# Kernel optimization log

Hardware: AMD Instinct MI355X
Metric: run time of the kernel (lower is better)

## Reference

```python
import jax, jax.numpy as jnp
import numpy as np

B, S, H, NH = 2, 2048, 2048, 16
HD = H // NH  # 128
ROPE_BASE = 10000.0


def rotate_half(x):
    x1, x2 = x[..., : x.shape[-1] // 2], x[..., x.shape[-1] // 2 :]
    return jnp.concatenate((-x2, x1), axis=-1)


def rope_cos_sin(seq_len, dim, dtype):
    inv_freq = 1.0 / (ROPE_BASE ** (jnp.arange(0, dim, 2, dtype=jnp.float32) / dim))
    t = jnp.arange(seq_len, dtype=jnp.float32)
    freqs = jnp.einsum('i,j->ij', t, inv_freq)          # [S, dim/2]
    emb = jnp.concatenate((freqs, freqs), axis=-1)       # [S, dim]
    return jnp.cos(emb).astype(dtype), jnp.sin(emb).astype(dtype)


def setup_inputs() -> dict:
    key = jax.random.key(0)
    ks = jax.random.split(key, 5)
    std = 1.0 / np.sqrt(H)
    return {
        'hidden_states': jax.random.normal(ks[0], (B, S, H), dtype=jnp.float32),
        'Wq': jax.random.normal(ks[1], (H, H), dtype=jnp.float32) * std,
        'Wk': jax.random.normal(ks[2], (H, H), dtype=jnp.float32) * std,
        'Wv': jax.random.normal(ks[3], (H, H), dtype=jnp.float32) * std,
        'Wo': jax.random.normal(ks[4], (H, H), dtype=jnp.float32) * std,
    }


def reference(hidden_states, Wq, Wk, Wv, Wo):
    bsz, q_len, _ = hidden_states.shape
    scale = 1.0 / np.sqrt(HD)
    # QKV projections (nn.Linear: x @ W.T)
    q = (hidden_states @ Wq.T).reshape(bsz, q_len, NH, HD).transpose(0, 2, 1, 3)
    k = (hidden_states @ Wk.T).reshape(bsz, q_len, NH, HD).transpose(0, 2, 1, 3)
    v = (hidden_states @ Wv.T).reshape(bsz, q_len, NH, HD).transpose(0, 2, 1, 3)
    # RoPE
    cos, sin = rope_cos_sin(q_len, HD, hidden_states.dtype)  # [S, HD]
    cos = cos[None, None]
    sin = sin[None, None]
    q = q * cos + rotate_half(q) * sin
    k = k * cos + rotate_half(k) * sin
    # attention (no mask, eval dropout = identity)
    attn = jnp.einsum('bhqd,bhkd->bhqk', q, k) * scale
    attn = jax.nn.softmax(attn.astype(jnp.float32), axis=-1).astype(q.dtype)
    out = jnp.einsum('bhqk,bhkd->bhqd', attn, v)
    out = out.transpose(0, 2, 1, 3).reshape(bsz, q_len, H)
    return out @ Wo.T
```

## Files before the change

kernel.cpp:

```cpp
#include <hip/hip_runtime.h>
#include <hip/hip_bf16.h>
#include <math.h>

#define Bb 2
#define Ss 2048
#define Hh 2048
#define NHh 16
#define HDd 128
#define Mm (Bb*Ss)

typedef __bf16 bf16;
typedef __bf16 bf16x8 __attribute__((ext_vector_type(8)));
typedef __bf16 bf16x4 __attribute__((ext_vector_type(4)));
typedef float  f32x4  __attribute__((ext_vector_type(4)));

#define MFMA16(a,b,c) __builtin_amdgcn_mfma_f32_16x16x32_bf16((a),(b),(c),0,0,0)

__device__ __forceinline__ void gll16(const void* g, void* l) {
  __builtin_amdgcn_global_load_lds((__attribute__((address_space(1))) void*)g,
                                   (__attribute__((address_space(3))) void*)l, 16, 0, 0);
}

__global__ __launch_bounds__(256) void k_tables(float* __restrict__ cosT, float* __restrict__ sinT) {
  int id = blockIdx.x * 256 + threadIdx.x;
  int s = id >> 6, j = id & 63;
  float inv = 1.0f / powf(10000.0f, (float)j * (1.0f/64.0f));
  float a = (float)s * inv;
  cosT[id] = cosf(a);
  sinT[id] = sinf(a);
}

__global__ __launch_bounds__(256) void k_cvt(const float* __restrict__ in, bf16* __restrict__ out) {
  size_t i = ((size_t)blockIdx.x * 256 + threadIdx.x) * 4;
  float4 v = *(const float4*)(in + i);
  bf16x4 r = { (bf16)v.x, (bf16)v.y, (bf16)v.z, (bf16)v.w };
  *(bf16x4*)(out + i) = r;
}

template<int EPI>
__global__ __launch_bounds__(256) void k_gemm(
    const bf16* __restrict__ A, const bf16* __restrict__ Bw,
    float* __restrict__ C, bf16* __restrict__ QKb, bf16* __restrict__ Vt,
    int M, int N, int K)
{
  __shared__ bf16 As[128*64];
  __shared__ bf16 Bs[128*64];
  const int tid = threadIdx.x;
  const int lane = tid & 63;
  const int w = tid >> 6, wm = w & 1, wn = w >> 1;
  const int cpx = gridDim.x >> 3;
  const int bid = (blockIdx.x & 7) * cpx + (blockIdx.x >> 3);
  const int mt = M >> 7;
  const int bm = bid % mt, bn = bid / mt;
  const int r8 = tid >> 3, c8 = tid & 7;
  const bf16* Ag = A  + (size_t)(bm*128 + r8) * K + c8*8;
  const bf16* Bg = Bw + (size_t)(bn*128 + r8) * K + c8*8;
  bf16* Asw = &As[r8*64 + c8*8];
  bf16* Bsw = &Bs[r8*64 + c8*8];

  f32x4 acc[4][4] = {};
  for (int k0 = 0; k0 < K; k0 += 64) {
#pragma unroll
    for (int i = 0; i < 4; ++i) {
      gll16(Ag + (size_t)i*32*K + k0, Asw + i*32*64);
      gll16(Bg + (size_t)i*32*K + k0, Bsw + i*32*64);
    }
    __syncthreads();
#pragma unroll
    for (int kc = 0; kc < 2; ++kc) {
      bf16x8 af[4], bfv[4];
#pragma unroll
      for (int mi = 0; mi < 4; ++mi)
        af[mi] = *(const bf16x8*)&As[(wm*64 + mi*16 + (lane & 15))*64 + kc*32 + (lane>>4)*8];
#pragma unroll
      for (int ni = 0; ni < 4; ++ni)
        bfv[ni] = *(const bf16x8*)&Bs[(wn*64 + ni*16 + (lane & 15))*64 + kc*32 + (lane>>4)*8];
#pragma unroll
      for (int mi = 0; mi < 4; ++mi)
#pragma unroll
        for (int ni = 0; ni < 4; ++ni)
          acc[mi][ni] = MFMA16(af[mi], bfv[ni], acc[mi][ni]);
    }
    __syncthreads();
  }
  const int colB = bn*128 + wn*64;
  if (EPI == 0) {
#pragma unroll
    for (int mi = 0; mi < 4; ++mi)
#pragma unroll
      for (int ni = 0; ni < 4; ++ni) {
        int row0 = bm*128 + wm*64 + mi*16 + (lane>>4)*4;
        int col  = colB + ni*16 + (lane & 15);
#pragma unroll
        for (int r = 0; r < 4; ++r)
          C[(size_t)(row0 + r) * N + col] = acc[mi][ni][r];
      }
  } else if (colB < 4096) {
#pragma unroll
    for (int mi = 0; mi < 4; ++mi)
#pragma unroll
      for (int ni = 0; ni < 4; ++ni) {
        int row0 = bm*128 + wm*64 + mi*16 + (lane>>4)*4;
        int col  = colB + ni*16 + (lane & 15);
#pragma unroll
        for (int r = 0; r < 4; ++r)
          QKb[(size_t)(row0 + r) * 4096 + col] = (bf16)acc[mi][ni][r];
      }
  } else {
#pragma unroll
    for (int mi = 0; mi < 4; ++mi)
#pragma unroll
      for (int ni = 0; ni < 4; ++ni) {
        int row0 = bm*128 + wm*64 + mi*16 + (lane>>4)*4;
        int n2   = colB + ni*16 + (lane & 15) - 4096;
        int b = row0 >> 11, s0 = row0 & (Ss-1);
        bf16x4 pk = { (bf16)acc[mi][ni][0], (bf16)acc[mi][ni][1],
                      (bf16)acc[mi][ni][2], (bf16)acc[mi][ni][3] };
        *(bf16x4*)&Vt[((size_t)(b*NHh + (n2>>7))*HDd + (n2&127))*Ss + s0] = pk;
      }
  }
}

__global__ __launch_bounds__(256) void k_rope(
    const bf16* __restrict__ QKb,
    const float* __restrict__ cosT, const float* __restrict__ sinT,
    bf16* __restrict__ Qb, bf16* __restrict__ Kb)
{
  const size_t id = (size_t)blockIdx.x * 256 + threadIdx.x;
  const int j = (int)(id & 63);
  const size_t row = id >> 6;
  const size_t tok = row >> 4;
  const int h = (int)(row & 15);
  const int s = (int)(tok & (Ss - 1));
  const float c = cosT[s*64 + j], sn = sinT[s*64 + j];
  const size_t qbase = tok * 4096 + h * 128;
  const float scale = 0.08838834764831845f;
  float q1 = (float)QKb[qbase + j],        q2 = (float)QKb[qbase + 64 + j];
  float k1 = (float)QKb[qbase + 2048 + j], k2 = (float)QKb[qbase + 2048 + 64 + j];
  const size_t obase = row * HDd;
  Qb[obase + j]      = (bf16)((q1*c - q2*sn) * scale);
  Qb[obase + 64 + j] = (bf16)((q2*c + q1*sn) * scale);
  Kb[obase + j]      = (bf16)(k1*c - k2*sn);
  Kb[obase + 64 + j] = (bf16)(k2*c + k1*sn);
}

__global__ __launch_bounds__(256) void k_attn(
    const bf16* __restrict__ Qb, const bf16* __restrict__ Kb,
    const bf16* __restrict__ Vt, bf16* __restrict__ Ob)
{
  __shared__ bf16 Ks[2][64*128];
  __shared__ bf16 Vs[2][128*64];
  __shared__ bf16 Ps[64*72];
  const int cpx = gridDim.x >> 3;
  const int blk = (blockIdx.x & 7) * cpx + (blockIdx.x >> 3);
  const int bh = blk >> 5;
  const int q0 = (blk & 31) * 64;
  const int b = bh >> 4, h = bh & 15;
  const int tid = threadIdx.x, lane = tid & 63, w = tid >> 6;

  const int rK = tid >> 4, cK = tid & 15;
  const int rV = tid >> 3, cV = tid & 7;
  const bf16* Kg0 = Kb + ((size_t)b*Ss*NHh + h) * HDd;
  const bf16* Vg0 = Vt + (size_t)bh * HDd * Ss;

  auto stage = [&](int bufi, int kv0) {
#pragma unroll
    for (int i = 0; i < 4; ++i) {
      const int rowK = i*16 + rK; const int sck = cK ^ (rowK & 7);
      gll16(Kg0 + (size_t)(kv0 + rowK)*(NHh*HDd) + sck*8, &Ks[bufi][rowK*128 + cK*8]);
      const int rowV = i*32 + rV; const int scv = cV ^ (rowV & 7);
      gll16(Vg0 + (size_t)rowV*Ss + kv0 + scv*8, &Vs[bufi][rowV*64 + cV*8]);
    }
  };

  bf16x8 aq[4];
  {
    const int qr = q0 + w*16 + (lane & 15);
    const bf16* qp = Qb + ((size_t)(b*Ss + qr) * NHh + h) * HDd + (lane>>4)*8;
#pragma unroll
    for (int kc = 0; kc < 4; ++kc) aq[kc] = *(const bf16x8*)(qp + kc*32);
  }
  float m_i[4], l_i[4];
  f32x4 o[8] = {};
#pragma unroll
  for (int i = 0; i < 4; ++i) { m_i[i] = -1e30f; l_i[i] = 0.f; }

  stage(0, 0);
  asm volatile("s_waitcnt vmcnt(0)" ::: "memory");
  __builtin_amdgcn_s_barrier();
  asm volatile("" ::: "memory");

  const int NT = Ss / 64;
  for (int t = 0; t < NT; ++t) {
    const int cur = t & 1;
    if (t + 1 < NT) stage(cur ^ 1, (t + 1) * 64);

    f32x4 sf[4];
    __builtin_amdgcn_s_setprio(1);
#pragma unroll
    for (int nf = 0; nf < 4; ++nf) {
      f32x4 a = {0.f,0.f,0.f,0.f};
#pragma unroll
      for (int kc = 0; kc < 4; ++kc) {
        const int row = nf*16 + (lane & 15);
        const int ch  = kc*4 + (lane>>4);
        bf16x8 bk = *(const bf16x8*)&Ks[cur][row*128 + (ch ^ (row & 7))*8];
        a = MFMA16(aq[kc], bk, a);
      }
      sf[nf] = a;
    }
    __builtin_amdgcn_s_setprio(0);

    float x4[4];
#pragma unroll
    for (int i = 0; i < 4; ++i) {
      float x = fmaxf(fmaxf(sf[0][i], sf[1][i]), fmaxf(sf[2][i], sf[3][i]));
      x = fmaxf(x, __shfl_xor(x, 1));
      x = fmaxf(x, __shfl_xor(x, 2));
      x = fmaxf(x, __shfl_xor(x, 4));
      x = fmaxf(x, __shfl_xor(x, 8));
      x4[i] = x;
    }
    bool grow = (x4[0] > m_i[0] + 8.f) || (x4[1] > m_i[1] + 8.f) ||
                (x4[2] > m_i[2] + 8.f) || (x4[3] > m_i[3] + 8.f);
    if (__any(grow)) {
#pragma unroll
      for (int i = 0; i < 4; ++i) {
        float mnew = fmaxf(m_i[i], x4[i]);
        float c = __expf(m_i[i] - mnew);
        m_i[i] = mnew; l_i[i] *= c;
#pragma unroll
        for (int nfo = 0; nfo < 8; ++nfo) o[nfo][i] *= c;
      }
    }
    float ps[4] = {0.f,0.f,0.f,0.f};
#pragma unroll
    for (int nf = 0; nf < 4; ++nf)
#pragma unroll
      for (int i = 0; i < 4; ++i) {
        float pv = __expf(sf[nf][i] - m_i[i]);
        sf[nf][i] = pv;
        ps[i] += pv;
      }
#pragma unroll
    for (int i = 0; i < 4; ++i) {
      float s = ps[i];
      s += __shfl_xor(s, 1); s += __shfl_xor(s, 2);
      s += __shfl_xor(s, 4); s += __shfl_xor(s, 8);
      l_i[i] += s;
    }
#pragma unroll
    for (int nf = 0; nf < 4; ++nf)
#pragma unroll
      for (int i = 0; i < 4; ++i)
        Ps[(w*16 + (lane>>4)*4 + i)*72 + nf*16 + (lane & 15)] = (bf16)sf[nf][i];

    __builtin_amdgcn_s_setprio(1);
#pragma unroll
    for (int kc = 0; kc < 2; ++kc) {
      bf16x8 pa = *(const bf16x8*)&Ps[(w*16 + (lane & 15))*72 + kc*32 + (lane>>4)*8];
#pragma unroll
      for (int nfo = 0; nfo < 8; ++nfo) {
        const int row = nfo*16 + (lane & 15);
        const int ch  = kc*4 + (lane>>4);
        bf16x8 bv = *(const bf16x8*)&Vs[cur][row*64 + (ch ^ (row & 7))*8];
        o[nfo] = MFMA16(pa, bv, o[nfo]);
      }
    }
    __builtin_amdgcn_s_setprio(0);

    asm volatile("s_waitcnt vmcnt(0)" ::: "memory");
    __builtin_amdgcn_s_barrier();
    asm volatile("" ::: "memory");
  }

#pragma unroll
  for (int nfo = 0; nfo < 8; ++nfo)
#pragma unroll
    for (int i = 0; i < 4; ++i) {
      const int qr = q0 + w*16 + (lane>>4)*4 + i;
      const int d  = nfo*16 + (lane & 15);
      Ob[((size_t)(b*Ss + qr) * NHh + h) * HDd + d] = (bf16)(o[nfo][i] / l_i[i]);
    }
}

extern "C" void kernel_launch(void* const* d_in, const int* in_sizes, int n_in,
                              void* d_out, int out_size, void* d_ws, size_t ws_size,
                              hipStream_t stream) {
  (void)in_sizes; (void)n_in; (void)out_size; (void)ws_size;
  const float* X  = (const float*)d_in[0];
  const float* Wq = (const float*)d_in[1];
  const float* Wk = (const float*)d_in[2];
  const float* Wv = (const float*)d_in[3];
  const float* Wo = (const float*)d_in[4];
  float* out = (float*)d_out;

  char* p = (char*)d_ws;
  size_t off = 0;
  auto take = [&](size_t bytes) { char* r = p + off; off += (bytes + 255) & ~(size_t)255; return r; };

  float* cosT = (float*)take((size_t)Ss*64*4);
  float* sinT = (float*)take((size_t)Ss*64*4);
  bf16*  Xb   = (bf16*) take((size_t)Mm*Hh*2);
  bf16*  Wqkv = (bf16*) take((size_t)3*Hh*Hh*2);
  bf16*  Wob  = (bf16*) take((size_t)Hh*Hh*2);
  bf16*  QKb  = (bf16*) take((size_t)Mm*4096*2);
  bf16*  Vt   = (bf16*) take((size_t)Mm*Hh*2);
  bf16*  Qb   = (bf16*) take((size_t)Mm*Hh*2);
  bf16*  Kb2  = (bf16*) take((size_t)Mm*Hh*2);
  bf16*  Ob   = (bf16*) take((size_t)Mm*Hh*2);

  k_tables<<<(Ss*64)/256, 256, 0, stream>>>(cosT, sinT);
  k_cvt<<<(Mm*Hh)/4/256, 256, 0, stream>>>(X,  Xb);
  k_cvt<<<(Hh*Hh)/4/256, 256, 0, stream>>>(Wq, Wqkv);
  k_cvt<<<(Hh*Hh)/4/256, 256, 0, stream>>>(Wk, Wqkv + (size_t)Hh*Hh);
  k_cvt<<<(Hh*Hh)/4/256, 256, 0, stream>>>(Wv, Wqkv + (size_t)2*Hh*Hh);
  k_cvt<<<(Hh*Hh)/4/256, 256, 0, stream>>>(Wo, Wob);

  k_gemm<1><<<(Mm/128) * (3*Hh/128), 256, 0, stream>>>(Xb, Wqkv, nullptr, QKb, Vt, Mm, 3*Hh, Hh);
  k_rope<<<((size_t)Mm*NHh*64)/256, 256, 0, stream>>>(QKb, cosT, sinT, Qb, Kb2);
  k_attn<<<Bb*NHh*(Ss/64), 256, 0, stream>>>(Qb, Kb2, Vt, Ob);
  k_gemm<0><<<(Mm/128) * (Hh/128), 256, 0, stream>>>(Ob, Wob, out, nullptr, nullptr, Mm, Hh, Hh);
}
```

Measured before the change: 534.8 us.

## Use exp2 softmax with log2e-folded scale and defer row-sum reductions

Folds log2(e) into the Q scaling so the attention softmax can use exp2f in place of __expf. Row sums are now kept as per-lane partial sums and reduced across lanes only once after the KV loop. The row-max shuffle reduction now runs only when the lazy rescale triggers, with a per-lane threshold scaled to the log2 domain. This removes most per-tile cross-lane shuffles and exponent scaling from the inner loop. The cost is that a lane's partial max can differ from the true row max, which leaves some risk in exponent range handling.

Result: faster. 501.8 us (-6.2%).

```diff
diff --git a/kernel.cpp b/kernel.cpp
--- a/kernel.cpp
+++ b/kernel.cpp
@@ -134,7 +134,7 @@
   const int s = (int)(tok & (Ss - 1));
   const float c = cosT[s*64 + j], sn = sinT[s*64 + j];
   const size_t qbase = tok * 4096 + h * 128;
-  const float scale = 0.08838834764831845f;
+  const float scale = 0.12753102543421936f;
   float q1 = (float)QKb[qbase + j],        q2 = (float)QKb[qbase + 64 + j];
   float k1 = (float)QKb[qbase + 2048 + j], k2 = (float)QKb[qbase + 2048 + 64 + j];
   const size_t obase = row * HDd;
@@ -180,10 +180,10 @@
 #pragma unroll
     for (int kc = 0; kc < 4; ++kc) aq[kc] = *(const bf16x8*)(qp + kc*32);
   }
-  float m_i[4], l_i[4];
+  float m_i[4], l_par[4];
   f32x4 o[8] = {};
 #pragma unroll
-  for (int i = 0; i < 4; ++i) { m_i[i] = -1e30f; l_i[i] = 0.f; }
+  for (int i = 0; i < 4; ++i) { m_i[i] = -1e30f; l_par[i] = 0.f; }
 
   stage(0, 0);
   asm volatile("s_waitcnt vmcnt(0)" ::: "memory");
@@ -211,44 +211,35 @@
     }
     __builtin_amdgcn_s_setprio(0);
 
-    float x4[4];
-#pragma unroll
-    for (int i = 0; i < 4; ++i) {
-      float x = fmaxf(fmaxf(sf[0][i], sf[1][i]), fmaxf(sf[2][i], sf[3][i]));
-      x = fmaxf(x, __shfl_xor(x, 1));
-      x = fmaxf(x, __shfl_xor(x, 2));
-      x = fmaxf(x, __shfl_xor(x, 4));
-      x = fmaxf(x, __shfl_xor(x, 8));
-      x4[i] = x;
-    }
-    bool grow = (x4[0] > m_i[0] + 8.f) || (x4[1] > m_i[1] + 8.f) ||
-                (x4[2] > m_i[2] + 8.f) || (x4[3] > m_i[3] + 8.f);
+    float xl[4];
+#pragma unroll
+    for (int i = 0; i < 4; ++i)
+      xl[i] = fmaxf(fmaxf(sf[0][i], sf[1][i]), fmaxf(sf[2][i], sf[3][i]));
+    bool grow = (xl[0] > m_i[0] + 11.5f) || (xl[1] > m_i[1] + 11.5f) ||
+                (xl[2] > m_i[2] + 11.5f) || (xl[3] > m_i[3] + 11.5f);
     if (__any(grow)) {
 #pragma unroll
       for (int i = 0; i < 4; ++i) {
-        float mnew = fmaxf(m_i[i], x4[i]);
-        float c = __expf(m_i[i] - mnew);
-        m_i[i] = mnew; l_i[i] *= c;
+        float x = xl[i];
+        x = fmaxf(x, __shfl_xor(x, 1));
+        x = fmaxf(x, __shfl_xor(x, 2));
+        x = fmaxf(x, __shfl_xor(x, 4));
+        x = fmaxf(x, __shfl_xor(x, 8));
+        float mnew = fmaxf(m_i[i], x);
+        float c = exp2f(m_i[i] - mnew);
+        m_i[i] = mnew; l_par[i] *= c;
 #pragma unroll
         for (int nfo = 0; nfo < 8; ++nfo) o[nfo][i] *= c;
       }
     }
-    float ps[4] = {0.f,0.f,0.f,0.f};
 #pragma unroll
     for (int nf = 0; nf < 4; ++nf)
 #pragma unroll
       for (int i = 0; i < 4; ++i) {
-        float pv = __expf(sf[nf][i] - m_i[i]);
+        float pv = exp2f(sf[nf][i] - m_i[i]);
         sf[nf][i] = pv;
-        ps[i] += pv;
-      }
-#pragma unroll
-    for (int i = 0; i < 4; ++i) {
-      float s = ps[i];
-      s += __shfl_xor(s, 1); s += __shfl_xor(s, 2);
-      s += __shfl_xor(s, 4); s += __shfl_xor(s, 8);
-      l_i[i] += s;
-    }
+        l_par[i] += pv;
+      }
 #pragma unroll
     for (int nf = 0; nf < 4; ++nf)
 #pragma unroll
@@ -274,13 +265,21 @@
     asm volatile("" ::: "memory");
   }
 
+  float linv[4];
+#pragma unroll
+  for (int i = 0; i < 4; ++i) {
+    float s = l_par[i];
+    s += __shfl_xor(s, 1); s += __shfl_xor(s, 2);
+    s += __shfl_xor(s, 4); s += __shfl_xor(s, 8);
+    linv[i] = 1.0f / s;
+  }
 #pragma unroll
   for (int nfo = 0; nfo < 8; ++nfo)
 #pragma unroll
     for (int i = 0; i < 4; ++i) {
       const int qr = q0 + w*16 + (lane>>4)*4 + i;
       const int d  = nfo*16 + (lane & 15);
-      Ob[((size_t)(b*Ss + qr) * NHh + h) * HDd + d] = (bf16)(o[nfo][i] / l_i[i]);
+      Ob[((size_t)(b*Ss + qr) * NHh + h) * HDd + d] = (bf16)(o[nfo][i] * linv[i]);
     }
 }
 
```
